# Kernel optimization log

Measured on AMD Instinct MI355X. Metric: run time of the kernel, lower is better.

Reference implementation:

```python
import jax, jax.numpy as jnp
import numpy as np

B, H, W, C = 2, 64, 64, 1024
L = H * W
HC, WC = 32, 32
NH, DH = 16, 64
NUM_REMAIN = 1638


def setup_inputs() -> dict:
    key = jax.random.key(0)
    ks = jax.random.split(key, 8)
    s = 1.0 / np.sqrt(C)
    x = jax.random.normal(ks[0], (B, L, C), jnp.float32)
    cached_x = jax.random.normal(ks[1], (B, HC, WC, C), jnp.float32)
    W_qkv = jax.random.normal(ks[2], (3 * C, C), jnp.float32) * s
    q_bias = jnp.zeros((C,), jnp.float32)
    v_bias = jnp.zeros((C,), jnp.float32)
    W_proj = jax.random.normal(ks[3], (C, C), jnp.float32) * s
    b_proj = jnp.zeros((C,), jnp.float32)
    scale_mul_log = jnp.full((1, NH, 1, 1), np.log(4.0), jnp.float32)
    # rope cache as (cos, sin) pairs over the flat token axis, DH//2 freqs
    ang = jax.random.uniform(ks[4], (L, DH // 2), jnp.float32) * (2 * np.pi)
    rope_grid = jnp.stack([jnp.cos(ang), jnp.sin(ang)], axis=0)  # (2, L, DH//2)
    return {"x": x, "cached_x": cached_x, "W_qkv": W_qkv, "q_bias": q_bias,
            "v_bias": v_bias, "W_proj": W_proj, "b_proj": b_proj,
            "scale_mul_log": scale_mul_log, "rope_grid": rope_grid,
            "num_remain": NUM_REMAIN}


def reference(x, cached_x, W_qkv, q_bias, v_bias, W_proj, b_proj,
              scale_mul_log, rope_grid, num_remain):
    Bx, Lx, Cx = x.shape
    # --- FastVAR token merge: MSE-to-spatial-mean selection (adaptive_avg_pool2d -> mean over L)
    mean_x = jnp.mean(x, axis=1, keepdims=True)                      # (B,1,C)
    mse = jnp.sum((x - mean_x) ** 2, axis=-1)                        # (B,L)
    idx = jnp.argsort(-mse, axis=1)[:, :num_remain]                  # (B,n) descending
    bix = jnp.arange(Bx)[:, None]
    xm = x[bix, idx]                                                 # (B,n,C) merged tokens
    # --- qkv projection with (q_bias, 0, v_bias)
    bias = jnp.concatenate([q_bias, jnp.zeros_like(q_bias), v_bias])
    qkv = (xm @ W_qkv.T + bias).reshape(Bx, -1, 3, NH, DH)
    qkv = qkv.transpose(2, 0, 3, 1, 4)                               # (3,B,H,n,dh)
    q, k, v = qkv[0], qkv[1], qkv[2]
    # --- cos attention: L2-normalize q,k; head-wise learned scale on q; sdpa scale = 1
    scale_mul = jnp.exp(jnp.minimum(scale_mul_log, jnp.log(100.0)))  # (1,NH,1,1)
    def l2n(t):
        return t / jnp.maximum(jnp.linalg.norm(t, axis=-1, keepdims=True), 1e-12)
    q = l2n(q) * scale_mul
    k = l2n(k)
    # --- 2D RoPE with per-sample gathered cache at the kept-token positions
    rc = rope_grid[:, idx, :]                                        # (2,B,n,DH//2)
    r0 = rc[0][:, None, :, :]                                        # (B,1,n,DH//2)
    r1 = rc[1][:, None, :, :]
    def rope(t):
        tp = t.reshape(*t.shape[:-1], DH // 2, 2)
        t0, t1 = tp[..., 0], tp[..., 1]
        return jnp.stack([r0 * t0 - r1 * t1, r1 * t0 + r0 * t1], axis=-1).reshape(t.shape)
    q = rope(q)
    k = rope(k)
    # --- attention over merged tokens
    attn = jax.nn.softmax(jnp.einsum('bhqd,bhkd->bhqk', q, k), axis=-1)
    o = jnp.einsum('bhqk,bhkd->bhqd', attn, v)                       # (B,H,n,dh)
    o = o.transpose(0, 2, 1, 3).reshape(Bx, -1, Cx)                  # (B,n,C)
    o = o @ W_proj.T + b_proj
    up = jnp.repeat(jnp.repeat(cached_x, 2, axis=1), 2, axis=2).reshape(Bx, Lx, Cx)
    out_full = up.at[bix, idx].set(o)
    return x + out_full
```

## Files before the change

kernel.cpp:

```cpp
#include <hip/hip_runtime.h>
#include <hip/hip_bf16.h>
#include <math.h>

#define BQ   2
#define LQ   4096
#define CQ   1024
#define NHQ  16
#define DHQ  64
#define KSEL 1638
#define KPAD 1664
#define MTOT (BQ*KSEL)
#define MPAD 3328

typedef short s16x8 __attribute__((ext_vector_type(8)));
typedef float fx4   __attribute__((ext_vector_type(4)));

#define MFMA16(a,b,c) __builtin_amdgcn_mfma_f32_16x16x32_bf16(a,b,c,0,0,0)

__device__ __forceinline__ float b2f(unsigned short u) {
  union { float f; unsigned int i; } cv; cv.i = ((unsigned int)u) << 16; return cv.f;
}
__device__ __forceinline__ unsigned short f2b(float f) {
  union { float f; unsigned int i; } cv; cv.f = f;
  unsigned int x = cv.i;
  return (unsigned short)((x + 0x7fffu + ((x >> 16) & 1u)) >> 16);
}
__device__ __forceinline__ unsigned int fbits(float f) {
  union { float f; unsigned int i; } cv; cv.f = f; return cv.i;
}
__device__ __forceinline__ void async16(const void* g, void* l) {
  __builtin_amdgcn_global_load_lds((const __attribute__((address_space(1))) void*)g,
                                   (__attribute__((address_space(3))) void*)l, 16, 0, 0);
}
__device__ __forceinline__ float fexp2(float x) {
#if __has_builtin(__builtin_amdgcn_exp2f)
  return __builtin_amdgcn_exp2f(x);
#else
  return __expf(x * 0.69314718055994531f);
#endif
}

__global__ __launch_bounds__(256) void k_cvt2(const float* __restrict__ wqkv,
                                              const float* __restrict__ wproj,
                                              unsigned short* __restrict__ wqb,
                                              unsigned short* __restrict__ wpb) {
  int i = blockIdx.x * 256 + threadIdx.x;
  const float* s; unsigned short* d; int off;
  if (i < 786432) { s = wqkv;  d = wqb; off = i; }
  else            { s = wproj; d = wpb; off = i - 786432; }
  float4 v = ((const float4*)s)[off];
  ushort4 o;
  o.x = f2b(v.x); o.y = f2b(v.y); o.z = f2b(v.z); o.w = f2b(v.w);
  ((ushort4*)d)[off] = o;
}

__global__ __launch_bounds__(256) void k_mean_part(const float* __restrict__ x,
                                                   double* __restrict__ part) {
  int bid = blockIdx.x;
  int cb = bid & 3, ch = (bid >> 2) & 31, b = bid >> 7;
  int c = cb * 256 + threadIdx.x;
  const float* p = x + ((size_t)b * LQ + (size_t)ch * 128) * CQ + c;
  double s = 0.0;
  for (int r = 0; r < 128; ++r) s += (double)p[(size_t)r * CQ];
  part[((size_t)b * 32 + ch) * CQ + c] = s;
}

__global__ __launch_bounds__(256) void k_mean_reduce(const double* __restrict__ part,
                                                     double* __restrict__ mean) {
  int g = blockIdx.x * 256 + threadIdx.x;
  int b = g >> 10, c = g & 1023;
  double s = 0.0;
  for (int ch = 0; ch < 32; ++ch) s += part[((size_t)b * 32 + ch) * CQ + c];
  mean[g] = s * (1.0 / 4096.0);
}

__global__ __launch_bounds__(256) void k_mse_base(const float* __restrict__ x,
                                                  const float* __restrict__ cached,
                                                  const double* __restrict__ mean,
                                                  double* __restrict__ mse,
                                                  float* __restrict__ out,
                                                  unsigned short* __restrict__ xb) {
  int bl = blockIdx.x; int b = bl >> 12, l = bl & 4095;
  int hh = l >> 6, ww = l & 63;
  size_t xoff = ((size_t)b * LQ + l) * CQ;
  size_t uoff = (((size_t)b * 32 + (hh >> 1)) * 32 + (ww >> 1)) * CQ;
  const double* mrow = mean + (size_t)b * CQ;
  int c0 = threadIdx.x * 4;
  float4 xv = *(const float4*)(x + xoff + c0);
  float4 uv = *(const float4*)(cached + uoff + c0);
  float4 ov;
  ov.x = xv.x + uv.x; ov.y = xv.y + uv.y; ov.z = xv.z + uv.z; ov.w = xv.w + uv.w;
  *(float4*)(out + xoff + c0) = ov;
  ushort4 xo;
  xo.x = f2b(xv.x); xo.y = f2b(xv.y); xo.z = f2b(xv.z); xo.w = f2b(xv.w);
  ((ushort4*)xb)[(xoff + c0) >> 2] = xo;
  double d0 = (double)xv.x - mrow[c0];
  double d1 = (double)xv.y - mrow[c0 + 1];
  double d2 = (double)xv.z - mrow[c0 + 2];
  double d3 = (double)xv.w - mrow[c0 + 3];
  double ss = d0 * d0 + d1 * d1 + d2 * d2 + d3 * d3;
  for (int o = 1; o < 64; o <<= 1) ss += __shfl_xor(ss, o);
  __shared__ double ws4[4];
  if ((threadIdx.x & 63) == 0) ws4[threadIdx.x >> 6] = ss;
  __syncthreads();
  if (threadIdx.x == 0) mse[(size_t)b * LQ + l] = ws4[0] + ws4[1] + ws4[2] + ws4[3];
}

__global__ __launch_bounds__(1024) void k_topk(const double* __restrict__ mse,
                                               int* __restrict__ idx_sel) {
  __shared__ unsigned long long u[4096];
  __shared__ unsigned int whist[16 * 257];
  __shared__ unsigned int wtot[4];
  __shared__ unsigned long long sh_prefix;
  __shared__ int sh_rem, sh_rem2, sh_bsel, sh_cnt, sh_eqcnt;
  __shared__ int eqbuf[256];
  int b = blockIdx.x, t = threadIdx.x;
  int wv = t >> 6, laneid = t & 63;
  for (int p = 0; p < 4; ++p) {
    int i = p * 1024 + t;
    u[i] = (unsigned long long)__double_as_longlong(mse[(size_t)b * LQ + i]);
  }
  if (t == 0) { sh_prefix = 0ULL; sh_rem = KSEL; sh_cnt = 0; sh_eqcnt = 0; }
  __syncthreads();
  for (int shift = 56; shift >= 0; shift -= 8) {
    for (int z = t; z < 16 * 257; z += 1024) whist[z] = 0u;
    __syncthreads();
    unsigned long long pref = sh_prefix;
#pragma unroll
    for (int p = 0; p < 4; ++p) {
      int i = p * 1024 + t;
      unsigned long long v = u[i];
      bool cand = (shift == 56) || ((v >> ((shift + 8) & 63)) == pref);
      if (cand) atomicAdd(&whist[wv * 257 + ((unsigned int)(v >> shift) & 255u)], 1u);
    }
    __syncthreads();
    unsigned int myc = 0, mysc = 0;
    if (t < 256) {
      unsigned int s = 0;
      int bin = 255 - t;
#pragma unroll
      for (int wvi = 0; wvi < 16; ++wvi) s += whist[wvi * 257 + bin];
      myc = s;
      mysc = myc;
#pragma unroll
      for (int o = 1; o < 64; o <<= 1) {
        unsigned int v2 = __shfl_up(mysc, o);
        if (laneid >= o) mysc += v2;
      }
      if (laneid == 63) wtot[wv] = mysc;
    }
    __syncthreads();
    if (t < 256) {
      unsigned int basep = 0;
      for (int wvi = 0; wvi < wv; ++wvi) basep += wtot[wvi];
      unsigned int incl = basep + mysc;
      unsigned int excl = incl - myc;
      unsigned int rem = (unsigned int)sh_rem;
      if (excl < rem && rem <= incl) {
        sh_bsel = 255 - t;
        sh_rem2 = (int)(rem - excl);
      }
    }
    __syncthreads();
    if (t == 0) {
      sh_prefix = (sh_prefix << 8) | (unsigned long long)sh_bsel;
      sh_rem = sh_rem2;
    }
    __syncthreads();
  }
  unsigned long long T = sh_prefix;
  int rem_eq = sh_rem;
#pragma unroll
  for (int p = 0; p < 4; ++p) {
    int i = p * 1024 + t;
    unsigned long long v = u[i];
    bool win = (v > T);
    unsigned long long mask = __ballot(win);
    int total = __popcll(mask);
    int base = 0;
    if (laneid == 0 && total > 0) base = atomicAdd(&sh_cnt, total);
    base = __shfl(base, 0);
    if (win) {
      int lpos = __popcll(mask & ((1ULL << laneid) - 1ULL));
      idx_sel[b * KPAD + base + lpos] = i;
    }
    if (v == T) {
      int e = atomicAdd(&sh_eqcnt, 1);
      if (e < 256) eqbuf[e] = i;
    }
  }
  __syncthreads();
  if (t == 0) {
    int n = sh_eqcnt; if (n > 256) n = 256;
    for (int a = 1; a < n; ++a) {
      int key = eqbuf[a]; int c = a - 1;
      while (c >= 0 && eqbuf[c] > key) { eqbuf[c + 1] = eqbuf[c]; --c; }
      eqbuf[c + 1] = key;
    }
    int base = sh_cnt;
    for (int a = 0; a < rem_eq && a < n; ++a) idx_sel[b * KPAD + base + a] = eqbuf[a];
    for (int a = KSEL; a < KPAD; ++a) idx_sel[b * KPAD + a] = 0;
  }
}

__global__ __launch_bounds__(256) void k_gemmA(const unsigned short* __restrict__ Asrc,
                                               const unsigned short* __restrict__ Bmat,
                                               const int* __restrict__ idx_sel,
                                               unsigned short* __restrict__ Cbf) {
  int bm = blockIdx.x % 26, bn = blockIdx.x / 26;
  int tid = threadIdx.x;
  int w = tid >> 6, lane = tid & 63, quad = lane >> 4, l15 = lane & 15;
  int wm = w & 1, wn = w >> 1;
  __shared__ __align__(16) unsigned char sm[2][16384];

  const unsigned short* gA[2];
  const unsigned short* gB[2];
#pragma unroll
  for (int p = 0; p < 2; ++p) {
    int e = p * 256 + tid; int row = e >> 2, kc = e & 3;
    int m = bm * 128 + row; if (m >= MTOT) m = MTOT - 1;
    int bb = m / KSEL; int ii = m - bb * KSEL;
    int lsel = idx_sel[bb * KPAD + ii];
    gA[p] = Asrc + ((size_t)bb * LQ + lsel) * CQ + kc * 8;
    gB[p] = Bmat + (size_t)(bn * 128 + row) * CQ + kc * 8;
  }

  fx4 acc[4][4];
#pragma unroll
  for (int a = 0; a < 4; ++a)
#pragma unroll
    for (int c = 0; c < 4; ++c) acc[a][c] = (fx4){0.f, 0.f, 0.f, 0.f};

#define STAGE_A(buf, it) do { int ke = (it) * 32;                                   \
    _Pragma("unroll")                                                               \
    for (int p = 0; p < 2; ++p) {                                                   \
      async16(gA[p] + ke, sm[buf] + p * 4096 + w * 1024);                           \
      async16(gB[p] + ke, sm[buf] + 8192 + p * 4096 + w * 1024);                    \
    } } while (0)

  STAGE_A(0, 0);
  for (int it = 0; it < 32; ++it) {
    int cur = it & 1;
    if (it < 31) STAGE_A(cur ^ 1, it + 1);
    if (it < 31) asm volatile("s_waitcnt vmcnt(4)");
    else         asm volatile("s_waitcnt vmcnt(0)");
    __builtin_amdgcn_s_barrier();
    const unsigned char* smb = sm[cur];
    s16x8 af[4], bf[4];
#pragma unroll
    for (int mt = 0; mt < 4; ++mt)
      af[mt] = *(const s16x8*)(smb + ((wm * 64 + mt * 16 + l15) * 64 + quad * 16));
#pragma unroll
    for (int nt = 0; nt < 4; ++nt)
      bf[nt] = *(const s16x8*)(smb + 8192 + ((wn * 64 + nt * 16 + l15) * 64 + quad * 16));
#pragma unroll
    for (int mt = 0; mt < 4; ++mt)
#pragma unroll
      for (int nt = 0; nt < 4; ++nt)
        acc[mt][nt] = MFMA16(af[mt], bf[nt], acc[mt][nt]);
    __builtin_amdgcn_s_barrier();
  }
#undef STAGE_A

#pragma unroll
  for (int mt = 0; mt < 4; ++mt)
#pragma unroll
    for (int nt = 0; nt < 4; ++nt) {
      int n = bn * 128 + wn * 64 + nt * 16 + l15;
      int mbase = bm * 128 + wm * 64 + mt * 16 + quad * 4;
      fx4 vv = acc[mt][nt];
#pragma unroll
      for (int r = 0; r < 4; ++r) {
        int m = mbase + r;
        if (m < MTOT) Cbf[(size_t)m * 3072 + n] = f2b(vv[r]);
      }
    }
}

__global__ __launch_bounds__(256) void k_gemmB(const unsigned short* __restrict__ Asrc,
                                               const unsigned short* __restrict__ Bmat,
                                               const int* __restrict__ idx_sel,
                                               float* __restrict__ Cf,
                                               const float* __restrict__ xin,
                                               const float* __restrict__ bproj) {
  int bid = blockIdx.x;
  int swz = (bid & 7) * 104 + (bid >> 3);
  int bm = swz % 52, bn = swz / 52;
  int tid = threadIdx.x;
  int w = tid >> 6, lane = tid & 63, quad = lane >> 4, l15 = lane & 15;
  int wm = w & 1, wn = w >> 1;
  __shared__ __align__(16) unsigned char sm[2][16384];

  const unsigned short* g4[4];
#pragma unroll
  for (int p = 0; p < 4; ++p) {
    int e = (p & 1) * 256 + tid; int row = e >> 3, kc = e & 7;
    if (p < 2) {
      int m = bm * 64 + row; if (m >= MTOT) m = MTOT - 1;
      int bb = m / KSEL; int ii = m - bb * KSEL;
      g4[p] = Asrc + ((size_t)bb * KPAD + ii) * CQ + kc * 8;
    } else {
      g4[p] = Bmat + (size_t)(bn * 64 + row) * CQ + kc * 8;
    }
  }

  fx4 acc[2][2];
#pragma unroll
  for (int a = 0; a < 2; ++a)
#pragma unroll
    for (int c = 0; c < 2; ++c) acc[a][c] = (fx4){0.f, 0.f, 0.f, 0.f};

#define STAGE_B(buf, it) do { int ke = (it) * 64;                                   \
    _Pragma("unroll")                                                               \
    for (int p = 0; p < 4; ++p)                                                     \
      async16(g4[p] + ke, sm[buf] + p * 4096 + w * 1024);                           \
    } while (0)

  STAGE_B(0, 0);
  for (int it = 0; it < 16; ++it) {
    int cur = it & 1;
    if (it < 15) STAGE_B(cur ^ 1, it + 1);
    if (it < 15) asm volatile("s_waitcnt vmcnt(4)");
    else         asm volatile("s_waitcnt vmcnt(0)");
    __builtin_amdgcn_s_barrier();
    const unsigned char* smb = sm[cur];
#pragma unroll
    for (int kk = 0; kk < 2; ++kk) {
      s16x8 af[2], bf2[2];
#pragma unroll
      for (int mt = 0; mt < 2; ++mt)
        af[mt] = *(const s16x8*)(smb + ((wm * 32 + mt * 16 + l15) * 64 + kk * 32 + quad * 8) * 2);
#pragma unroll
      for (int nt = 0; nt < 2; ++nt)
        bf2[nt] = *(const s16x8*)(smb + 8192 + ((wn * 32 + nt * 16 + l15) * 64 + kk * 32 + quad * 8) * 2);
#pragma unroll
      for (int mt = 0; mt < 2; ++mt)
#pragma unroll
        for (int nt = 0; nt < 2; ++nt)
          acc[mt][nt] = MFMA16(af[mt], bf2[nt], acc[mt][nt]);
    }
    __builtin_amdgcn_s_barrier();
  }
#undef STAGE_B

#pragma unroll
  for (int mt = 0; mt < 2; ++mt)
#pragma unroll
    for (int nt = 0; nt < 2; ++nt) {
      int n = bn * 64 + wn * 32 + nt * 16 + l15;
      int mbase = bm * 64 + wm * 32 + mt * 16 + quad * 4;
      fx4 vv = acc[mt][nt];
      float bp = bproj[n];
#pragma unroll
      for (int r = 0; r < 4; ++r) {
        int m = mbase + r;
        if (m < MTOT) {
          int bb = m / KSEL; int ii = m - bb * KSEL;
          int lsel = idx_sel[bb * KPAD + ii];
          size_t off = ((size_t)bb * LQ + lsel) * CQ + n;
          Cf[off] = xin[off] + vv[r] + bp;
        }
      }
    }
}

__global__ __launch_bounds__(256) void k_normrope(const unsigned short* __restrict__ qkv,
                                                  const int* __restrict__ idx_sel,
                                                  const float* __restrict__ qbias,
                                                  const float* __restrict__ vbias,
                                                  const float* __restrict__ sml,
                                                  const float* __restrict__ rope,
                                                  unsigned short* __restrict__ qo,
                                                  unsigned short* __restrict__ ko,
                                                  unsigned short* __restrict__ vt) {
  int bid = blockIdx.x;
  int tile = bid % 26; int h = (bid / 26) & 15; int b = bid / (26 * 16);
  int tid = threadIdx.x; int w = tid >> 6; int d = tid & 63;
  __shared__ unsigned short vtile[64 * 68];
  float scale = expf(fminf(sml[h], 4.6051702f)) * 1.4426950408889634f;
  float qb = qbias[h * 64 + d];
  float vb = vbias[h * 64 + d];
  for (int pass = 0; pass < 16; ++pass) {
    int il = pass * 4 + w;
    int i = tile * 64 + il;
    float vraw = 0.f;
    if (i < KSEL) {
      int lsel = idx_sel[b * KPAD + i];
      size_t base = ((size_t)(b * KSEL + i)) * 3072 + h * 64 + d;
      int tt = d >> 1;
      float r0 = rope[(size_t)lsel * 32 + tt];
      float r1 = rope[(size_t)LQ * 32 + (size_t)lsel * 32 + tt];
      float qv = b2f(qkv[base]) + qb;
      float ss = qv * qv;
      for (int o = 1; o < 64; o <<= 1) ss += __shfl_xor(ss, o);
      float qn = qv / fmaxf(sqrtf(ss), 1e-12f) * scale;
      float qp = __shfl_xor(qn, 1);
      float qr = (d & 1) ? (r1 * qp + r0 * qn) : (r0 * qn - r1 * qp);
      qo[((size_t)(b * NHQ + h) * KPAD + i) * 64 + d] = f2b(qr);
      float kv = b2f(qkv[base + 1024]);
      float ks = kv * kv;
      for (int o = 1; o < 64; o <<= 1) ks += __shfl_xor(ks, o);
      float kn = kv / fmaxf(sqrtf(ks), 1e-12f);
      float kp = __shfl_xor(kn, 1);
      float kr = (d & 1) ? (r1 * kp + r0 * kn) : (r0 * kn - r1 * kp);
      ko[((size_t)(b * NHQ + h) * KPAD + i) * 64 + d] = f2b(kr);
      vraw = b2f(qkv[base + 2048]) + vb;
    }
    vtile[d * 68 + il] = f2b(vraw);
  }
  __syncthreads();
  int row = tid >> 2, c0 = (tid & 3) * 16;
  s16x8 o0, o1;
#pragma unroll
  for (int jj = 0; jj < 8; ++jj) {
    o0[jj] = (short)vtile[row * 68 + c0 + jj];
    o1[jj] = (short)vtile[row * 68 + c0 + 8 + jj];
  }
  size_t doff = ((size_t)((b * NHQ + h) * 64 + row)) * KPAD + (size_t)tile * 64 + c0;
  *(s16x8*)(vt + doff) = o0;
  *(s16x8*)(vt + doff + 8) = o1;
}

__global__ __launch_bounds__(256, 4) void k_attn(const unsigned short* __restrict__ qb,
                                                 const unsigned short* __restrict__ kb,
                                                 const unsigned short* __restrict__ vtb,
                                                 const float* __restrict__ sml,
                                                 unsigned short* __restrict__ pO,
                                                 float* __restrict__ pl) {
  int qt = blockIdx.x; int bh = blockIdx.y; int part = blockIdx.z;
  int b = bh >> 4, h = bh & 15;
  int t0 = part * 13, t1 = t0 + 13;
  int q0 = qt * 128;
  int tid = threadIdx.x, w = tid >> 6, lane = tid & 63, quad = lane >> 4, l15 = lane & 15;
  float M = __expf(fminf(sml[h], 4.6051702f)) * 1.4426950408889634f;
  __shared__ __align__(16) unsigned short Kt[64 * 72];
  __shared__ __align__(16) unsigned short Vt[64 * 72];
  __shared__ __align__(16) unsigned short Pq[4][32 * 72];
  unsigned short* Pw = Pq[w];
  const unsigned short* qbase = qb + (size_t)(b * NHQ + h) * KPAD * 64;
  const unsigned short* kbase = kb + (size_t)(b * NHQ + h) * KPAD * 64;
  const unsigned short* vbase = vtb + (size_t)(b * NHQ + h) * 64 * KPAD;

  int r0 = tid >> 3, c0 = tid & 7;
  int r1 = 32 + r0, c1 = c0;

  s16x8 qf[2][2];
#pragma unroll
  for (int qtile = 0; qtile < 2; ++qtile)
#pragma unroll
    for (int kb2 = 0; kb2 < 2; ++kb2) {
      int row = q0 + w * 32 + qtile * 16 + l15;
      qf[qtile][kb2] = *(const s16x8*)(qbase + (size_t)row * 64 + kb2 * 32 + quad * 8);
    }

  float lsum[2] = {0.f, 0.f};
  fx4 oacc[2][4];
#pragma unroll
  for (int qtile = 0; qtile < 2; ++qtile)
#pragma unroll
    for (int dt = 0; dt < 4; ++dt) oacc[qtile][dt] = (fx4){0.f, 0.f, 0.f, 0.f};

  s16x8 kn0, kn1, vn0, vn1;
  {
    int j0 = t0 * 64;
    kn0 = *(const s16x8*)(kbase + (size_t)(j0 + r0) * 64 + c0 * 8);
    kn1 = *(const s16x8*)(kbase + (size_t)(j0 + r1) * 64 + c1 * 8);
    vn0 = *(const s16x8*)(vbase + (size_t)r0 * KPAD + j0 + c0 * 8);
    vn1 = *(const s16x8*)(vbase + (size_t)r1 * KPAD + j0 + c1 * 8);
  }

  for (int t = t0; t < t1; ++t) {
    int j0 = t * 64;
    bool tail = (j0 + 64 > KSEL);
    __builtin_amdgcn_s_barrier();
    *(s16x8*)(Kt + r0 * 72 + c0 * 8) = kn0;
    *(s16x8*)(Kt + r1 * 72 + c1 * 8) = kn1;
    *(s16x8*)(Vt + r0 * 72 + c0 * 8) = vn0;
    *(s16x8*)(Vt + r1 * 72 + c1 * 8) = vn1;
    if (t + 1 < t1) {
      int jn = (t + 1) * 64;
      kn0 = *(const s16x8*)(kbase + (size_t)(jn + r0) * 64 + c0 * 8);
      kn1 = *(const s16x8*)(kbase + (size_t)(jn + r1) * 64 + c1 * 8);
      vn0 = *(const s16x8*)(vbase + (size_t)r0 * KPAD + jn + c0 * 8);
      vn1 = *(const s16x8*)(vbase + (size_t)r1 * KPAD + jn + c1 * 8);
    }
    asm volatile("s_waitcnt lgkmcnt(0)" ::: "memory");
    __builtin_amdgcn_s_barrier();

    fx4 sacc[2][4];
#pragma unroll
    for (int qtile = 0; qtile < 2; ++qtile)
#pragma unroll
      for (int jj = 0; jj < 4; ++jj) sacc[qtile][jj] = (fx4){0.f, 0.f, 0.f, 0.f};
    __builtin_amdgcn_s_setprio(1);
#pragma unroll
    for (int jj = 0; jj < 4; ++jj) {
      int jl = jj * 16 + l15;
      s16x8 kf0 = *(const s16x8*)(Kt + jl * 72 + quad * 8);
      s16x8 kf1 = *(const s16x8*)(Kt + jl * 72 + 32 + quad * 8);
      sacc[0][jj] = MFMA16(kf0, qf[0][0], sacc[0][jj]);
      sacc[1][jj] = MFMA16(kf0, qf[1][0], sacc[1][jj]);
      sacc[0][jj] = MFMA16(kf1, qf[0][1], sacc[0][jj]);
      sacc[1][jj] = MFMA16(kf1, qf[1][1], sacc[1][jj]);
    }
    __builtin_amdgcn_s_setprio(0);
#pragma unroll
    for (int qtile = 0; qtile < 2; ++qtile)
#pragma unroll
      for (int jj = 0; jj < 4; ++jj) {
        int jbase = j0 + jj * 16 + quad * 4;
        fx4 sv = sacc[qtile][jj];
        float p0 = fexp2(sv[0] - M);
        float p1 = fexp2(sv[1] - M);
        float p2 = fexp2(sv[2] - M);
        float p3 = fexp2(sv[3] - M);
        if (tail) {
          if (jbase + 0 >= KSEL) p0 = 0.f;
          if (jbase + 1 >= KSEL) p1 = 0.f;
          if (jbase + 2 >= KSEL) p2 = 0.f;
          if (jbase + 3 >= KSEL) p3 = 0.f;
        }
        lsum[qtile] += (p0 + p1) + (p2 + p3);
        unsigned int lo = (fbits(p1) & 0xffff0000u) | (fbits(p0) >> 16);
        unsigned int hi = (fbits(p3) & 0xffff0000u) | (fbits(p2) >> 16);
        *(uint2*)(Pw + (qtile * 16 + l15) * 72 + jj * 16 + quad * 4) =
            make_uint2(lo, hi);
      }
    __builtin_amdgcn_s_setprio(1);
#pragma unroll
    for (int js = 0; js < 2; ++js) {
      s16x8 pf0 = *(const s16x8*)(Pw + l15 * 72 + js * 32 + quad * 8);
      s16x8 pf1 = *(const s16x8*)(Pw + (16 + l15) * 72 + js * 32 + quad * 8);
#pragma unroll
      for (int dt = 0; dt < 4; ++dt) {
        s16x8 vf = *(const s16x8*)(Vt + (dt * 16 + l15) * 72 + js * 32 + quad * 8);
        oacc[0][dt] = MFMA16(pf0, vf, oacc[0][dt]);
        oacc[1][dt] = MFMA16(pf1, vf, oacc[1][dt]);
      }
    }
    __builtin_amdgcn_s_setprio(0);
  }

#pragma unroll
  for (int qtile = 0; qtile < 2; ++qtile) {
    float s = lsum[qtile];
    s += __shfl_xor(s, 16);
    s += __shfl_xor(s, 32);
    lsum[qtile] = s;
  }

  size_t pbase = (((size_t)part * 2 + b) * NHQ + h) * KPAD;
#pragma unroll
  for (int qtile = 0; qtile < 2; ++qtile) {
    int gqb = q0 + w * 32 + qtile * 16;
    if (quad == 0) pl[pbase + gqb + l15] = lsum[qtile];
  }

#pragma unroll
  for (int qtile = 0; qtile < 2; ++qtile)
#pragma unroll
    for (int dt = 0; dt < 4; ++dt)
#pragma unroll
      for (int r = 0; r < 4; ++r)
        Pw[(qtile * 16 + quad * 4 + r) * 72 + dt * 16 + l15] = f2b(oacc[qtile][dt][r]);
#pragma unroll
  for (int pass = 0; pass < 4; ++pass) {
    int row = pass * 8 + (lane >> 3), chunk = lane & 7;
    s16x8 vv = *(const s16x8*)(Pw + row * 72 + chunk * 8);
    *(s16x8*)(pO + (pbase + q0 + w * 32 + row) * 64 + chunk * 8) = vv;
  }
}

__global__ __launch_bounds__(256) void k_comb(const unsigned short* __restrict__ pO,
                                              const float* __restrict__ pl,
                                              unsigned short* __restrict__ ob) {
  size_t g = (size_t)blockIdx.x * 256 + threadIdx.x;
  int d = (int)(g & 63);
  size_t row = g >> 6;
  int gq = (int)(row % KPAD);
  int bhh = (int)(row / KPAD);
  int b = bhh >> 4, h = bhh & 15;
  float oa = b2f(pO[g]);
  float obv = b2f(pO[g + 3407872]);
  float la = pl[row], lb = pl[row + 53248];
  float o = (oa + obv) / (la + lb);
  ob[((size_t)(b * KPAD + gq)) * CQ + h * 64 + d] = f2b(o);
}

extern "C" void kernel_launch(void* const* d_in, const int* in_sizes, int n_in,
                              void* d_out, int out_size, void* d_ws, size_t ws_size,
                              hipStream_t stream) {
  const float* x      = (const float*)d_in[0];
  const float* cached = (const float*)d_in[1];
  const float* wqkv   = (const float*)d_in[2];
  const float* qbias  = (const float*)d_in[3];
  const float* vbias  = (const float*)d_in[4];
  const float* wproj  = (const float*)d_in[5];
  const float* bproj  = (const float*)d_in[6];
  const float* sml    = (const float*)d_in[7];
  const float* rope   = (const float*)d_in[8];
  float* out = (float*)d_out;
  char* ws = (char*)d_ws;

  double* meanpart        = (double*)(ws);
  double* mean            = (double*)(ws + 524288);
  double* mse             = (double*)(ws + 540672);
  int* idx_sel            = (int*)(ws + 606208);
  unsigned short* x_bf    = (unsigned short*)(ws + 619520);
  unsigned short* wqkv_bf = (unsigned short*)(ws + 17396736);
  unsigned short* qkv     = (unsigned short*)(ws + 23688192);
  unsigned short* pO      = (unsigned short*)(ws + 619520);
  float* pl               = (float*)(ws + 14251008);
  unsigned short* wproj_bf= (unsigned short*)(ws + 44135424);
  unsigned short* qo      = (unsigned short*)(ws + 46232576);
  unsigned short* ko      = (unsigned short*)(ws + 53048320);
  unsigned short* vt      = (unsigned short*)(ws + 59864064);
  unsigned short* ob      = (unsigned short*)(ws + 66679808);

  hipLaunchKernelGGL(k_cvt2, dim3(4096), dim3(256), 0, stream, wqkv, wproj,
                     wqkv_bf, wproj_bf);
  hipLaunchKernelGGL(k_mean_part, dim3(256), dim3(256), 0, stream, x, meanpart);
  hipLaunchKernelGGL(k_mean_reduce, dim3(8), dim3(256), 0, stream, meanpart, mean);
  hipLaunchKernelGGL(k_mse_base, dim3(8192), dim3(256), 0, stream, x, cached, mean, mse,
                     out, x_bf);
  hipLaunchKernelGGL(k_topk, dim3(BQ), dim3(1024), 0, stream, mse, idx_sel);
  hipLaunchKernelGGL(k_gemmA, dim3(26 * 24), dim3(256), 0, stream,
                     x_bf, wqkv_bf, idx_sel, qkv);
  hipLaunchKernelGGL(k_normrope, dim3(26 * 16 * BQ), dim3(256), 0, stream,
                     qkv, idx_sel, qbias, vbias, sml, rope, qo, ko, vt);
  hipLaunchKernelGGL(k_attn, dim3(13, BQ * NHQ, 2), dim3(256), 0, stream,
                     qo, ko, vt, sml, pO, pl);
  hipLaunchKernelGGL(k_comb, dim3(13312), dim3(256), 0, stream, pO, pl, ob);
  hipLaunchKernelGGL(k_gemmB, dim3(832), dim3(256), 0, stream,
                     ob, wproj_bf, idx_sel, out, x, bproj);
}
```

Measured before the change: 289.2 us.

## Fold weight conversion into top-k launch, triple-buffer QKV GEMM, pack bf16 with cvt

Moves the fp32-to-bf16 weight conversion into extra blocks of the top-k kernel so it runs alongside the two-block selection and saves a launch. Deepens the QKV GEMM LDS pipeline from two to three stages with adjusted waitcnts and raises wave priority around the MFMA block. Replaces manual truncating bf16 packing of softmax probabilities with the hardware packed convert instruction. Risks: larger LDS per GEMM block may lower occupancy, and the fused conversion blocks carry the top-k kernel's large shared-memory footprint.

```diff
diff --git a/kernel.cpp b/kernel.cpp
--- a/kernel.cpp
+++ b/kernel.cpp
@@ -28,6 +28,11 @@
 __device__ __forceinline__ unsigned int fbits(float f) {
   union { float f; unsigned int i; } cv; cv.f = f; return cv.i;
 }
+__device__ __forceinline__ unsigned int cvtpk_bf16(float a, float b) {
+  unsigned int r;
+  asm("v_cvt_pk_bf16_f32 %0, %1, %2" : "=v"(r) : "v"(a), "v"(b));
+  return r;
+}
 __device__ __forceinline__ void async16(const void* g, void* l) {
   __builtin_amdgcn_global_load_lds((const __attribute__((address_space(1))) void*)g,
                                    (__attribute__((address_space(3))) void*)l, 16, 0, 0);
@@ -38,20 +43,6 @@
 #else
   return __expf(x * 0.69314718055994531f);
 #endif
-}
-
-__global__ __launch_bounds__(256) void k_cvt2(const float* __restrict__ wqkv,
-                                              const float* __restrict__ wproj,
-                                              unsigned short* __restrict__ wqb,
-                                              unsigned short* __restrict__ wpb) {
-  int i = blockIdx.x * 256 + threadIdx.x;
-  const float* s; unsigned short* d; int off;
-  if (i < 786432) { s = wqkv;  d = wqb; off = i; }
-  else            { s = wproj; d = wpb; off = i - 786432; }
-  float4 v = ((const float4*)s)[off];
-  ushort4 o;
-  o.x = f2b(v.x); o.y = f2b(v.y); o.z = f2b(v.z); o.w = f2b(v.w);
-  ((ushort4*)d)[off] = o;
 }
 
 __global__ __launch_bounds__(256) void k_mean_part(const float* __restrict__ x,
@@ -107,7 +98,22 @@
 }
 
 __global__ __launch_bounds__(1024) void k_topk(const double* __restrict__ mse,
-                                               int* __restrict__ idx_sel) {
+                                               int* __restrict__ idx_sel,
+                                               const float* __restrict__ wqkv,
+                                               const float* __restrict__ wproj,
+                                               unsigned short* __restrict__ wqb,
+                                               unsigned short* __restrict__ wpb) {
+  if (blockIdx.x >= 2) {
+    int i = (blockIdx.x - 2) * 1024 + threadIdx.x;
+    const float* s; unsigned short* d; int off;
+    if (i < 786432) { s = wqkv;  d = wqb; off = i; }
+    else            { s = wproj; d = wpb; off = i - 786432; }
+    float4 v = ((const float4*)s)[off];
+    ushort4 o;
+    o.x = f2b(v.x); o.y = f2b(v.y); o.z = f2b(v.z); o.w = f2b(v.w);
+    ((ushort4*)d)[off] = o;
+    return;
+  }
   __shared__ unsigned long long u[4096];
   __shared__ unsigned int whist[16 * 257];
   __shared__ unsigned int wtot[4];
@@ -211,7 +217,7 @@
   int tid = threadIdx.x;
   int w = tid >> 6, lane = tid & 63, quad = lane >> 4, l15 = lane & 15;
   int wm = w & 1, wn = w >> 1;
-  __shared__ __align__(16) unsigned char sm[2][16384];
+  __shared__ __align__(16) unsigned char sm[3][16384];
 
   const unsigned short* gA[2];
   const unsigned short* gB[2];
@@ -231,21 +237,23 @@
 #pragma unroll
     for (int c = 0; c < 4; ++c) acc[a][c] = (fx4){0.f, 0.f, 0.f, 0.f};
 
-#define STAGE_A(buf, it) do { int ke = (it) * 32;                                   \
+#define STAGE_A(boff, it) do { int ke = (it) * 32;                                  \
     _Pragma("unroll")                                                               \
     for (int p = 0; p < 2; ++p) {                                                   \
-      async16(gA[p] + ke, sm[buf] + p * 4096 + w * 1024);                           \
-      async16(gB[p] + ke, sm[buf] + 8192 + p * 4096 + w * 1024);                    \
+      async16(gA[p] + ke, sm[0] + (boff) + p * 4096 + w * 1024);                    \
+      async16(gB[p] + ke, sm[0] + (boff) + 8192 + p * 4096 + w * 1024);             \
     } } while (0)
 
   STAGE_A(0, 0);
+  STAGE_A(16384, 1);
   for (int it = 0; it < 32; ++it) {
-    int cur = it & 1;
-    if (it < 31) STAGE_A(cur ^ 1, it + 1);
-    if (it < 31) asm volatile("s_waitcnt vmcnt(4)");
-    else         asm volatile("s_waitcnt vmcnt(0)");
+    int cur = it % 3;
+    if (it + 2 < 32) STAGE_A(((it + 2) % 3) * 16384, it + 2);
+    if (it <= 29)      asm volatile("s_waitcnt vmcnt(8)");
+    else if (it == 30) asm volatile("s_waitcnt vmcnt(4)");
+    else               asm volatile("s_waitcnt vmcnt(0)");
     __builtin_amdgcn_s_barrier();
-    const unsigned char* smb = sm[cur];
+    const unsigned char* smb = sm[0] + cur * 16384;
     s16x8 af[4], bf[4];
 #pragma unroll
     for (int mt = 0; mt < 4; ++mt)
@@ -253,11 +261,13 @@
 #pragma unroll
     for (int nt = 0; nt < 4; ++nt)
       bf[nt] = *(const s16x8*)(smb + 8192 + ((wn * 64 + nt * 16 + l15) * 64 + quad * 16));
+    __builtin_amdgcn_s_setprio(1);
 #pragma unroll
     for (int mt = 0; mt < 4; ++mt)
 #pragma unroll
       for (int nt = 0; nt < 4; ++nt)
         acc[mt][nt] = MFMA16(af[mt], bf[nt], acc[mt][nt]);
+    __builtin_amdgcn_s_setprio(0);
     __builtin_amdgcn_s_barrier();
   }
 #undef STAGE_A
@@ -521,10 +531,8 @@
           if (jbase + 3 >= KSEL) p3 = 0.f;
         }
         lsum[qtile] += (p0 + p1) + (p2 + p3);
-        unsigned int lo = (fbits(p1) & 0xffff0000u) | (fbits(p0) >> 16);
-        unsigned int hi = (fbits(p3) & 0xffff0000u) | (fbits(p2) >> 16);
         *(uint2*)(Pw + (qtile * 16 + l15) * 72 + jj * 16 + quad * 4) =
-            make_uint2(lo, hi);
+            make_uint2(cvtpk_bf16(p0, p1), cvtpk_bf16(p2, p3));
       }
     __builtin_amdgcn_s_setprio(1);
 #pragma unroll
@@ -617,13 +625,12 @@
   unsigned short* vt      = (unsigned short*)(ws + 59864064);
   unsigned short* ob      = (unsigned short*)(ws + 66679808);
 
-  hipLaunchKernelGGL(k_cvt2, dim3(4096), dim3(256), 0, stream, wqkv, wproj,
-                     wqkv_bf, wproj_bf);
   hipLaunchKernelGGL(k_mean_part, dim3(256), dim3(256), 0, stream, x, meanpart);
   hipLaunchKernelGGL(k_mean_reduce, dim3(8), dim3(256), 0, stream, meanpart, mean);
   hipLaunchKernelGGL(k_mse_base, dim3(8192), dim3(256), 0, stream, x, cached, mean, mse,
                      out, x_bf);
-  hipLaunchKernelGGL(k_topk, dim3(BQ), dim3(1024), 0, stream, mse, idx_sel);
+  hipLaunchKernelGGL(k_topk, dim3(2 + 1024), dim3(1024), 0, stream, mse, idx_sel,
+                     wqkv, wproj, wqkv_bf, wproj_bf);
   hipLaunchKernelGGL(k_gemmA, dim3(26 * 24), dim3(256), 0, stream,
                      x_bf, wqkv_bf, idx_sel, qkv);
   hipLaunchKernelGGL(k_normrope, dim3(26 * 16 * BQ), dim3(256), 0, stream,
```

New measurement: 282.7 us. -2.2%, faster.
